# Performance work log

Hardware: AMD Instinct MI355X
Metric: run time of the kernel (lower is better)

Reference implementation:

```python
import jax, jax.numpy as jnp
import numpy as np

B, T, IMG = 64, 20, 64
IN_DIM = IMG * IMG          # 4096, from x.view(B,-1,64*64)
C_IN = 8                    # input_channels
R_DIM = C_IN * 1024         # 8192, reshape(B,20,-1,32,32) constraint
NF = 64                     # num_filters
Z_DIM = 256
LIN_IN = 2 * NF * 7 * 7     # 6272


def setup_inputs() -> dict:
    key = jax.random.key(0)
    ks = jax.random.split(key, 10)
    x = jax.random.normal(ks[0], (B, T, IMG, IMG), jnp.float32)
    Win = jax.random.normal(ks[1], (IN_DIM, R_DIM), jnp.float32) / np.sqrt(IN_DIM).astype(np.float32)
    U = jax.random.normal(ks[2], (IN_DIM, R_DIM), jnp.float32) / np.sqrt(IN_DIM).astype(np.float32)
    Wr = jax.random.normal(ks[3], (R_DIM, R_DIM), jnp.float32) / np.sqrt(R_DIM).astype(np.float32)
    conv1_w = jax.random.normal(ks[4], (NF, C_IN, 3, 3, 3), jnp.float32) * 0.05
    conv1_b = jax.random.normal(ks[5], (NF,), jnp.float32) * 0.01
    conv2_w = jax.random.normal(ks[6], (2 * NF, NF, 3, 4, 4), jnp.float32) * 0.05
    conv2_b = jax.random.normal(ks[7], (2 * NF,), jnp.float32) * 0.01
    lin_w = jax.random.normal(ks[8], (Z_DIM, LIN_IN), jnp.float32) * 0.02
    lin_b = jax.random.normal(ks[9], (Z_DIM,), jnp.float32) * 0.01
    return {"x": x, "Win": Win, "U": U, "Wr": Wr,
            "conv1_w": conv1_w, "conv1_b": conv1_b,
            "conv2_w": conv2_w, "conv2_b": conv2_b,
            "lin_w": lin_w, "lin_b": lin_b}


def reference(x, Win, U, Wr, conv1_w, conv1_b, conv2_w, conv2_b, lin_w, lin_b):
    Bn = x.shape[0]
    xf = x.reshape(Bn, T, IN_DIM)                      # (B,T,4096)
    h0 = jnp.tanh(xf[:, 0] @ Win)                      # (B,R)
    xU = jnp.einsum('bti,ir->tbr', xf[:, 1:], U)       # precompute input drive (T-1,B,R)

    def step(h, xu):
        h = jnp.tanh(xu + h @ Wr)
        return h, h

    _, hs = jax.lax.scan(step, h0, xU)                 # (T-1,B,R)
    H = jnp.concatenate([h0[None], hs], axis=0)        # (T,B,R)
    H = jnp.swapaxes(H, 0, 1)                          # (B,T,R)

    h = H.reshape(Bn, T, C_IN, 32, 32).transpose(0, 2, 1, 3, 4)  # (B,C,T,32,32)
    dn = ('NCDHW', 'OIDHW', 'NCDHW')
    y = jax.lax.conv_general_dilated(h, conv1_w, (1, 2, 2),
                                     [(1, 1), (1, 1), (1, 1)], dimension_numbers=dn)
    y = y + conv1_b[None, :, None, None, None]
    y = jax.nn.leaky_relu(y, 0.01)                     # (B,NF,20,16,16)
    y = jax.lax.conv_general_dilated(y, conv2_w, (1, 2, 2),
                                     [(1, 1), (0, 0), (0, 0)], dimension_numbers=dn)
    y = y + conv2_b[None, :, None, None, None]
    y = jax.nn.leaky_relu(y, 0.01)                     # (B,2NF,20,7,7)

    y = y.reshape(Bn, -1, T, LIN_IN)                   # (B,1,20,6272), same row-major view as torch
    y = y @ lin_w.T + lin_b                            # (B,1,20,Z_DIM)
    mu, log_var = jnp.split(y, 2, axis=3)
    return mu, log_var
```

## Files before the change

kernel.cpp:

```cpp
#include <hip/hip_runtime.h>

typedef __bf16 v8bf __attribute__((ext_vector_type(8)));
typedef float  v4f  __attribute__((ext_vector_type(4)));
typedef unsigned short us8 __attribute__((ext_vector_type(8)));

__device__ __forceinline__ float bf2f(unsigned short u) {
    union { unsigned int i; float f; } v; v.i = ((unsigned int)u) << 16; return v.f;
}
__device__ __forceinline__ unsigned short f2bf(float f) {
    union { float f; unsigned int i; } v; v.f = f;
    return (unsigned short)((v.i + 0x7fffu + ((v.i >> 16) & 1u)) >> 16);
}
__device__ __forceinline__ int sw(int b) { return b ^ (((b >> 7) & 7) << 4); }

__global__ __launch_bounds__(256)
void transpose_f32_bf16(const float* __restrict__ src,
                        unsigned short* __restrict__ dst, int K, int N)
{
    __shared__ unsigned short tile[64][72];
    const int tid = threadIdx.x;
    const int c0 = blockIdx.x * 64, r0 = blockIdx.y * 64;
    const int tr = tid >> 2, tc4 = tid & 3;
    const float* sp = src + (size_t)(r0 + tr) * N + c0 + tc4 * 16;
#pragma unroll
    for (int j = 0; j < 4; ++j) {
        v4f f = *reinterpret_cast<const v4f*>(sp + j * 4);
#pragma unroll
        for (int e = 0; e < 4; ++e) tile[tr][tc4 * 16 + j * 4 + e] = f2bf(f[e]);
    }
    __syncthreads();
    const int ow = tid >> 3, och = tid & 7;
#pragma unroll
    for (int p = 0; p < 2; ++p) {
        int orow = p * 32 + ow;
        us8 o;
#pragma unroll
        for (int e = 0; e < 8; ++e) o[e] = tile[och * 8 + e][orow];
        *reinterpret_cast<us8*>(dst + (size_t)(c0 + orow) * K + r0 + och * 8) = o;
    }
}

__global__ __launch_bounds__(256)
void cvt_x(const float* __restrict__ x, unsigned short* __restrict__ xb)
{
    int i = blockIdx.x * 256 + threadIdx.x;
    if (i >= 655360) return;
    v4f f0 = *reinterpret_cast<const v4f*>(x + (size_t)i * 8);
    v4f f1 = *reinterpret_cast<const v4f*>(x + (size_t)i * 8 + 4);
    us8 o;
#pragma unroll
    for (int e = 0; e < 4; ++e) { o[e] = f2bf(f0[e]); o[4 + e] = f2bf(f1[e]); }
    *reinterpret_cast<us8*>(xb + (size_t)i * 8) = o;
}

template<int BN, bool STORE_BF16, bool AF32, bool BF32>
__global__ __launch_bounds__(256, 2)
void gemm_bt(const void* __restrict__ Ap, int lda_lo, int lda_hi,
             const void* __restrict__ BTp, int ldb,
             void* __restrict__ Cout, int ldc,
             int ksub, long long csplit_stride)
{
    constexpr int FN  = BN / 32;
    constexpr int BCH = BN / 32;
    const int tid = threadIdx.x;
    const int lane = tid & 63, wid = tid >> 6;
    const int wr = wid >> 1, wc = wid & 1;
    const int nt = blockIdx.x, mt = blockIdx.y, kz = blockIdx.z;
    const int n0 = nt * BN;
    const int kstart = kz * ksub;

    __shared__ unsigned short smem[(64 + BN) * 64];
    char* As = reinterpret_cast<char*>(smem);
    char* Bs = reinterpret_cast<char*>(smem + 64 * 64);

    const unsigned short* A16 = (const unsigned short*)Ap;
    const float*          A32 = (const float*)Ap;
    const unsigned short* B16 = (const unsigned short*)BTp;
    const float*          B32 = (const float*)BTp;

    const int arow = AF32 ? (tid >> 2) : (tid >> 3);
    const int aq   = AF32 ? (tid & 3) : (tid & 7);
    const float* Ab32 = A32 + (size_t)arow * lda_lo + (size_t)mt * lda_hi + kstart + aq * 16;
    const unsigned short* Ab16 = A16 + (size_t)arow * lda_lo + (size_t)mt * lda_hi + kstart + aq * 8;
    const int brow = tid >> 3, bq = tid & 7;
    const float* Bb32 = B32 + (size_t)(n0 + brow) * ldb + kstart + bq * 8;
    const unsigned short* Bb16 = B16 + (size_t)(n0 + brow) * ldb + kstart + bq * 8;

    v4f fa[4];
    us8 ra[2];
    v4f fb[BCH][2];
    us8 rb[BCH];

    auto load = [&](int kk) {
        if (AF32) {
#pragma unroll
            for (int j = 0; j < 4; ++j)
                fa[j] = *reinterpret_cast<const v4f*>(Ab32 + kk + j * 4);
        } else {
#pragma unroll
            for (int p = 0; p < 2; ++p)
                ra[p] = *reinterpret_cast<const us8*>(Ab16 + (size_t)(p * 32) * lda_lo + kk);
        }
        if (BF32) {
#pragma unroll
            for (int p = 0; p < BCH; ++p) {
                fb[p][0] = *reinterpret_cast<const v4f*>(Bb32 + (size_t)(p * 32) * ldb + kk);
                fb[p][1] = *reinterpret_cast<const v4f*>(Bb32 + (size_t)(p * 32) * ldb + kk + 4);
            }
        } else {
#pragma unroll
            for (int p = 0; p < BCH; ++p)
                rb[p] = *reinterpret_cast<const us8*>(Bb16 + (size_t)(p * 32) * ldb + kk);
        }
    };
    auto stage = [&]() {
        if (AF32) {
#pragma unroll
            for (int h = 0; h < 2; ++h) {
                us8 v;
#pragma unroll
                for (int e = 0; e < 8; ++e) v[e] = f2bf(fa[h * 2 + (e >> 2)][e & 3]);
                *reinterpret_cast<us8*>(As + arow * 128 + (((aq * 2 + h) * 16) ^ ((arow & 7) << 4))) = v;
            }
        } else {
#pragma unroll
            for (int p = 0; p < 2; ++p)
                *reinterpret_cast<us8*>(As + (arow + p * 32) * 128 + ((aq * 16) ^ ((arow & 7) << 4))) = ra[p];
        }
#pragma unroll
        for (int p = 0; p < BCH; ++p) {
            us8 v;
            if (BF32) {
#pragma unroll
                for (int e = 0; e < 8; ++e) v[e] = f2bf(fb[p][e >> 2][e & 3]);
            } else v = rb[p];
            *reinterpret_cast<us8*>(Bs + (brow + p * 32) * 128 + ((bq * 16) ^ ((brow & 7) << 4))) = v;
        }
    };

    v4f z4 = {0.f, 0.f, 0.f, 0.f};
    v4f acc[2][FN];
#pragma unroll
    for (int i = 0; i < 2; ++i)
#pragma unroll
        for (int j = 0; j < FN; ++j) acc[i][j] = z4;

    const int l15 = lane & 15, l4 = lane >> 4;
    const int nk = ksub / 64;
    load(0);
    for (int it = 0; it < nk; ++it) {
        __syncthreads();
        stage();
        __syncthreads();
        if (it + 1 < nk) load((it + 1) * 64);
#pragma unroll
        for (int ks = 0; ks < 2; ++ks) {
            const int kb = (ks * 32 + l4 * 8) * 2;
            v8bf af[2], bfr[FN];
#pragma unroll
            for (int fm = 0; fm < 2; ++fm) {
                int row = wr * 32 + fm * 16 + l15;
                af[fm] = *reinterpret_cast<const v8bf*>(As + row * 128 + (kb ^ ((row & 7) << 4)));
            }
#pragma unroll
            for (int fn = 0; fn < FN; ++fn) {
                int row = wc * (BN / 2) + fn * 16 + l15;
                bfr[fn] = *reinterpret_cast<const v8bf*>(Bs + row * 128 + (kb ^ ((row & 7) << 4)));
            }
#pragma unroll
            for (int fm = 0; fm < 2; ++fm)
#pragma unroll
                for (int fn = 0; fn < FN; ++fn)
                    acc[fm][fn] = __builtin_amdgcn_mfma_f32_16x16x32_bf16(af[fm], bfr[fn], acc[fm][fn], 0, 0, 0);
        }
    }
    const long long m0 = (long long)mt * 64;
#pragma unroll
    for (int fm = 0; fm < 2; ++fm)
#pragma unroll
        for (int fn = 0; fn < FN; ++fn)
#pragma unroll
            for (int r = 0; r < 4; ++r) {
                long long row = m0 + wr * 32 + fm * 16 + l4 * 4 + r;
                long long col = n0 + wc * (BN / 2) + fn * 16 + l15;
                long long idx = (long long)kz * csplit_stride + row * ldc + col;
                if (STORE_BF16) reinterpret_cast<unsigned short*>(Cout)[idx] = f2bf(acc[fm][fn][r]);
                else            reinterpret_cast<float*>(Cout)[idx]          = acc[fm][fn][r];
            }
}

#define KZ 4
__global__ __launch_bounds__(256, 2)
void scan_step(const unsigned short* __restrict__ A, int lda,
               const unsigned short* __restrict__ BT, int ldb,
               int kper,
               const unsigned short* __restrict__ xu,
               unsigned short* __restrict__ hnext,
               unsigned short* __restrict__ Hbf, int t,
               float* __restrict__ part,
               unsigned int* __restrict__ tickets)
{
    const int tid = threadIdx.x, lane = tid & 63, wid = tid >> 6;
    const int wr = wid >> 1, wc = wid & 1;
    const int nt = blockIdx.x & 127, kz = blockIdx.x >> 7;
    const int n0 = nt * 64, kstart = kz * kper;
    const int l15 = lane & 15, l4 = lane >> 4;
    const int nit = kper >> 6;

    __shared__ unsigned short smem[32768];
    char* base = reinterpret_cast<char*>(smem);

    const int srow = tid >> 3, sq = tid & 7;
    const int gslot = sq ^ (srow & 7);
    const unsigned short* Asrc = A + (size_t)srow * lda + kstart + gslot * 8;
    const unsigned short* Bsrc = BT + (size_t)(n0 + srow) * ldb + kstart + gslot * 8;

    auto stage = [&](int buf, int kk) {
        char* dA = base + buf * 16384 + wid * 1024;
        char* dB = dA + 8192;
#pragma unroll
        for (int p = 0; p < 2; ++p) {
            __builtin_amdgcn_global_load_lds(
                (const __attribute__((address_space(1))) void*)(Asrc + kk + (size_t)p * 32 * lda),
                (__attribute__((address_space(3))) void*)(dA + p * 4096), 16, 0, 0);
            __builtin_amdgcn_global_load_lds(
                (const __attribute__((address_space(1))) void*)(Bsrc + kk + (size_t)p * 32 * ldb),
                (__attribute__((address_space(3))) void*)(dB + p * 4096), 16, 0, 0);
        }
    };

    v4f acc00 = {0.f, 0.f, 0.f, 0.f};
    v4f acc01 = acc00, acc10 = acc00, acc11 = acc00;

    stage(0, 0); stage(1, 64); stage(2, 128);
    for (int it = 0; it < nit; ++it) {
        const int ahead = nit - 1 - it;
        if (ahead >= 2)      asm volatile("s_waitcnt vmcnt(8)" ::: "memory");
        else if (ahead == 1) asm volatile("s_waitcnt vmcnt(4)" ::: "memory");
        else                 asm volatile("s_waitcnt vmcnt(0)" ::: "memory");
        __builtin_amdgcn_s_barrier();
        __builtin_amdgcn_sched_barrier(0);
        if (it + 3 < nit) stage((it + 3) & 3, (it + 3) * 64);
        const char* As = base + (it & 3) * 16384;
        const char* Bs = As + 8192;
#pragma unroll
        for (int ks = 0; ks < 2; ++ks) {
            const int kb = (ks * 32 + l4 * 8) * 2;
            v8bf a0, a1, b0, b1;
            { int row = wr * 32 + l15;      a0 = *reinterpret_cast<const v8bf*>(As + row * 128 + (kb ^ ((row & 7) << 4))); }
            { int row = wr * 32 + 16 + l15; a1 = *reinterpret_cast<const v8bf*>(As + row * 128 + (kb ^ ((row & 7) << 4))); }
            { int row = wc * 32 + l15;      b0 = *reinterpret_cast<const v8bf*>(Bs + row * 128 + (kb ^ ((row & 7) << 4))); }
            { int row = wc * 32 + 16 + l15; b1 = *reinterpret_cast<const v8bf*>(Bs + row * 128 + (kb ^ ((row & 7) << 4))); }
            acc00 = __builtin_amdgcn_mfma_f32_16x16x32_bf16(a0, b0, acc00, 0, 0, 0);
            acc01 = __builtin_amdgcn_mfma_f32_16x16x32_bf16(a0, b1, acc01, 0, 0, 0);
            acc10 = __builtin_amdgcn_mfma_f32_16x16x32_bf16(a1, b0, acc10, 0, 0, 0);
            acc11 = __builtin_amdgcn_mfma_f32_16x16x32_bf16(a1, b1, acc11, 0, 0, 0);
        }
    }

    float* mypart = part + (size_t)kz * 524288;
#pragma unroll
    for (int r = 0; r < 4; ++r) {
        int row0 = wr * 32 + l4 * 4 + r;
        int col0 = n0 + wc * 32 + l15;
        mypart[(size_t)row0 * 8192 + col0]             = acc00[r];
        mypart[(size_t)row0 * 8192 + col0 + 16]        = acc01[r];
        mypart[(size_t)(row0 + 16) * 8192 + col0]      = acc10[r];
        mypart[(size_t)(row0 + 16) * 8192 + col0 + 16] = acc11[r];
    }

    __shared__ int lastflag;
    __syncthreads();
    if (tid == 0) {
        unsigned int old = __hip_atomic_fetch_add(&tickets[nt], 1u,
                              __ATOMIC_ACQ_REL, __HIP_MEMORY_SCOPE_AGENT);
        lastflag = (old == KZ - 1);
    }
    __syncthreads();
    if (!lastflag) return;

    const int row = tid >> 2;
    const int c0 = n0 + (tid & 3) * 16;
    float pre[16];
    if (xu) {
        const us8* xp = reinterpret_cast<const us8*>(xu + (size_t)row * 8192 + c0);
        us8 x0 = xp[0], x1 = xp[1];
#pragma unroll
        for (int j = 0; j < 8; ++j) { pre[j] = bf2f(x0[j]); pre[8 + j] = bf2f(x1[j]); }
    } else {
#pragma unroll
        for (int j = 0; j < 16; ++j) pre[j] = 0.f;
    }
#pragma unroll
    for (int z = 0; z < KZ; ++z) {
        const float* pp = part + (size_t)z * 524288 + (size_t)row * 8192 + c0;
#pragma unroll
        for (int q = 0; q < 4; ++q) {
            v4f v = *reinterpret_cast<const v4f*>(pp + q * 4);
#pragma unroll
            for (int e = 0; e < 4; ++e) pre[q * 4 + e] += v[e];
        }
    }
    us8 o0, o1;
#pragma unroll
    for (int j = 0; j < 16; ++j) {
        unsigned short hb = f2bf(tanhf(pre[j]));
        if (j < 8) o0[j] = hb; else o1[j - 8] = hb;
        int col = c0 + j;
        Hbf[(((size_t)row * 20 + t) * 1024 + (col & 1023)) * 8 + (col >> 10)] = hb;
    }
    *reinterpret_cast<us8*>(hnext + (size_t)row * 8192 + c0)     = o0;
    *reinterpret_cast<us8*>(hnext + (size_t)row * 8192 + c0 + 8) = o1;
    if (tid == 0)
        __hip_atomic_store(&tickets[nt], 0u, __ATOMIC_RELAXED, __HIP_MEMORY_SCOPE_AGENT);
}

__global__ __launch_bounds__(256)
void cvt_w1(const float* __restrict__ w, unsigned short* __restrict__ o,
            unsigned int* __restrict__ tickets)
{
    if (blockIdx.x == 0 && threadIdx.x < 128) tickets[threadIdx.x] = 0;
    int idx = blockIdx.x * 256 + threadIdx.x;
    if (idx >= 64 * 224) return;
    int co = idx / 224, k = idx % 224;
    int g = k >> 3, ci = k & 7;
    float v = 0.f;
    if (g < 27) {
        int dt = g / 9, rr = g % 9, dy = rr / 3, dx = rr % 3;
        v = w[(((co * 8 + ci) * 3 + dt) * 3 + dy) * 3 + dx];
    }
    o[idx] = f2bf(v);
}
__global__ __launch_bounds__(256)
void cvt_w2(const float* __restrict__ w, unsigned short* __restrict__ o)
{
    int idx = blockIdx.x * 256 + threadIdx.x;
    if (idx >= 128 * 3072) return;
    int co = idx / 3072, k = idx % 3072;
    int g = k >> 6, ci = k & 63;
    int dt = g >> 4, dy = (g >> 2) & 3, dx = g & 3;
    o[idx] = f2bf(w[(((co * 64 + ci) * 3 + dt) * 4 + dy) * 4 + dx]);
}

__global__ __launch_bounds__(256, 2)
void conv1_kernel(const unsigned short* __restrict__ H,
                  const unsigned short* __restrict__ w1,
                  const float* __restrict__ bias,
                  unsigned short* __restrict__ y1)
{
    const int b = blockIdx.x, t = blockIdx.y;
    const int tid = threadIdx.x, lane = tid & 63, wid = tid >> 6;
    __shared__ unsigned short in_s[3 * 33 * 33 * 8];
    __shared__ unsigned short w_s[64 * 224];

    for (int i = tid; i < 13068; i += 256) reinterpret_cast<unsigned int*>(in_s)[i] = 0;
    __syncthreads();
    for (int idx = tid; idx < 3 * 1024; idx += 256) {
        int dt = idx >> 10, rem = idx & 1023;
        int iy = rem >> 5, ix = rem & 31;
        int ts = t + dt - 1;
        if (ts >= 0 && ts < 20) {
            us8 v = *reinterpret_cast<const us8*>(H + (((size_t)b * 20 + ts) * 1024 + rem) * 8);
            int byte = ((dt * 33 + iy + 1) * 33 + (ix + 1)) * 16;
            *reinterpret_cast<us8*>(reinterpret_cast<char*>(in_s) + sw(byte)) = v;
        }
    }
    for (int idx = tid; idx < 64 * 28; idx += 256) {
        int co = idx / 28, j = idx % 28;
        us8 v = *reinterpret_cast<const us8*>(w1 + co * 224 + j * 8);
        *reinterpret_cast<us8*>(reinterpret_cast<char*>(w_s) + sw(co * 448 + j * 16)) = v;
    }
    __syncthreads();

    const int l15 = lane & 15, l4 = lane >> 4;
    const int m_lo = wid * 64 + l15;
    v4f z4 = {0.f, 0.f, 0.f, 0.f};
    v4f acc[4][4];
#pragma unroll
    for (int i = 0; i < 4; ++i)
#pragma unroll
        for (int j = 0; j < 4; ++j) acc[i][j] = z4;

#pragma unroll
    for (int ks = 0; ks < 7; ++ks) {
        int g = ks * 4 + l4;
        int gc = g < 27 ? g : 26;
        int dt = gc / 9, rr = gc % 9, dy = rr / 3, dx = rr % 3;
        v8bf ap[4], aw[4];
#pragma unroll
        for (int fm = 0; fm < 4; ++fm) {
            int m = fm * 16 + m_lo;
            int py = m >> 4, px = m & 15;
            int byte = ((dt * 33 + 2 * py + dy) * 33 + 2 * px + dx) * 16;
            ap[fm] = *reinterpret_cast<const v8bf*>(reinterpret_cast<const char*>(in_s) + sw(byte));
        }
        int kb2 = (ks * 32 + l4 * 8) * 2;
#pragma unroll
        for (int fc = 0; fc < 4; ++fc) {
            int co = fc * 16 + l15;
            aw[fc] = *reinterpret_cast<const v8bf*>(reinterpret_cast<const char*>(w_s) + sw(co * 448 + kb2));
        }
#pragma unroll
        for (int fm = 0; fm < 4; ++fm)
#pragma unroll
            for (int fc = 0; fc < 4; ++fc)
                acc[fm][fc] = __builtin_amdgcn_mfma_f32_16x16x32_bf16(ap[fm], aw[fc], acc[fm][fc], 0, 0, 0);
    }
#pragma unroll
    for (int fm = 0; fm < 4; ++fm)
#pragma unroll
        for (int fc = 0; fc < 4; ++fc)
#pragma unroll
            for (int r = 0; r < 4; ++r) {
                int m  = wid * 64 + fm * 16 + l4 * 4 + r;
                int co = fc * 16 + l15;
                float v = acc[fm][fc][r] + bias[co];
                v = v > 0.f ? v : 0.01f * v;
                y1[(((size_t)b * 20 + t) * 256 + m) * 64 + co] = f2bf(v);
            }
}

__global__ __launch_bounds__(512, 2)
void conv2_kernel(const unsigned short* __restrict__ y1,
                  const unsigned short* __restrict__ w2,
                  const float* __restrict__ bias,
                  unsigned short* __restrict__ y2)
{
    const int b = blockIdx.x, t = blockIdx.y;
    const int tid = threadIdx.x, lane = tid & 63, wid = tid >> 6;
    const int wc = wid >> 1, wr = wid & 1;
    __shared__ unsigned short in_s[256 * 64];
    __shared__ unsigned short w_s[128 * 128];
    const int l15 = lane & 15, l4 = lane >> 4;

    const int m0v = wr * 32 + l15, m1v = m0v + 16;
    const int m0c = m0v < 49 ? m0v : 48, m1c = m1v < 49 ? m1v : 48;
    const int py0 = m0c / 7, px0 = m0c - py0 * 7;
    const int py1 = m1c / 7, px1 = m1c - py1 * 7;

    v4f acc[2][2];
#pragma unroll
    for (int i = 0; i < 2; ++i)
#pragma unroll
        for (int j = 0; j < 2; ++j) acc[i][j] = (v4f){0.f, 0.f, 0.f, 0.f};

    for (int dt = 0; dt < 3; ++dt) {
        int ts = t + dt - 1;
        __syncthreads();
        if (ts < 0 || ts >= 20) continue;
#pragma unroll
        for (int p = 0; p < 4; ++p) {
            int idx = tid + p * 512;
            int slot = idx >> 3, c8 = idx & 7;
            int yy = slot >> 4, xx = slot & 15;
            us8 v = *reinterpret_cast<const us8*>(y1 + (((size_t)b * 20 + ts) * 256 + slot) * 64 + c8 * 8);
            int cell = ((yy & 1) * 2 + (xx & 1)) * 64 + (yy >> 1) * 8 + (xx >> 1);
            int byte = cell * 128 + ((c8 * 16) ^ (((cell ^ (cell >> 3)) & 7) << 4));
            *reinterpret_cast<us8*>(reinterpret_cast<char*>(in_s) + byte) = v;
        }
        for (int kc = 0; kc < 8; ++kc) {
            __syncthreads();
#pragma unroll
            for (int p = 0; p < 4; ++p) {
                int idx = tid + p * 512;
                int co = idx >> 4, j = idx & 15;
                us8 v = *reinterpret_cast<const us8*>(w2 + (size_t)co * 3072 + dt * 1024 + kc * 128 + j * 8);
                *reinterpret_cast<us8*>(reinterpret_cast<char*>(w_s) + co * 256 + ((j * 16) ^ ((co & 7) << 4))) = v;
            }
            __syncthreads();
#pragma unroll
            for (int ks = 0; ks < 4; ++ks) {
                int klocal = ks * 32 + l4 * 8;
                int kk = kc * 128 + klocal;
                int dy = (kk >> 8) & 3, dx = (kk >> 6) & 3, ci0 = kk & 63;
                v8bf aw[2], bp[2];
#pragma unroll
                for (int fc = 0; fc < 2; ++fc) {
                    int co = wc * 32 + fc * 16 + l15;
                    aw[fc] = *reinterpret_cast<const v8bf*>(reinterpret_cast<const char*>(w_s)
                               + co * 256 + ((klocal * 2) ^ ((co & 7) << 4)));
                }
                int plane = ((dy & 1) << 1) | (dx & 1);
                int c0 = plane * 64 + (py0 + (dy >> 1)) * 8 + px0 + (dx >> 1);
                int c1 = plane * 64 + (py1 + (dy >> 1)) * 8 + px1 + (dx >> 1);
                bp[0] = *reinterpret_cast<const v8bf*>(reinterpret_cast<const char*>(in_s)
                          + c0 * 128 + ((ci0 * 2) ^ (((c0 ^ (c0 >> 3)) & 7) << 4)));
                bp[1] = *reinterpret_cast<const v8bf*>(reinterpret_cast<const char*>(in_s)
                          + c1 * 128 + ((ci0 * 2) ^ (((c1 ^ (c1 >> 3)) & 7) << 4)));
#pragma unroll
                for (int fc = 0; fc < 2; ++fc)
#pragma unroll
                    for (int fm = 0; fm < 2; ++fm)
                        acc[fc][fm] = __builtin_amdgcn_mfma_f32_16x16x32_bf16(aw[fc], bp[fm], acc[fc][fm], 0, 0, 0);
            }
        }
    }
#pragma unroll
    for (int fc = 0; fc < 2; ++fc)
#pragma unroll
        for (int fm = 0; fm < 2; ++fm)
#pragma unroll
            for (int r = 0; r < 4; ++r) {
                int co = wc * 32 + fc * 16 + l4 * 4 + r;
                int m  = wr * 32 + fm * 16 + l15;
                if (m < 49) {
                    float v = acc[fc][fm][r] + bias[co];
                    v = v > 0.f ? v : 0.01f * v;
                    y2[(((size_t)b * 128 + co) * 20 + t) * 49 + m] = f2bf(v);
                }
            }
}

__global__ __launch_bounds__(256)
void lin_epi(const float* __restrict__ linC, const float* __restrict__ lb,
             float* __restrict__ out)
{
    int i = blockIdx.x * 256 + threadIdx.x;
    int m = i >> 8, n = i & 255;
    float v = lb[n];
#pragma unroll
    for (int z = 0; z < 7; ++z) v += linC[(size_t)z * 327680 + i];
    size_t o = (n < 128) ? ((size_t)m * 128 + n) : (163840 + (size_t)m * 128 + (n - 128));
    out[o] = v;
}

extern "C" void kernel_launch(void* const* d_in, const int* in_sizes, int n_in,
                              void* d_out, int out_size, void* d_ws, size_t ws_size,
                              hipStream_t stream)
{
    const float* x   = (const float*)d_in[0];
    const float* Win = (const float*)d_in[1];
    const float* U   = (const float*)d_in[2];
    const float* Wr  = (const float*)d_in[3];
    const float* c1w = (const float*)d_in[4];
    const float* c1b = (const float*)d_in[5];
    const float* c2w = (const float*)d_in[6];
    const float* c2b = (const float*)d_in[7];
    const float* lw  = (const float*)d_in[8];
    const float* lb  = (const float*)d_in[9];

    char* ws = (char*)d_ws;
    unsigned short* WrT  = (unsigned short*)(ws);
    unsigned short* xbf  = (unsigned short*)(ws);
    unsigned short* WT   = (unsigned short*)(ws + 134217728ll);
    unsigned short* y1   = (unsigned short*)(ws + 134217728ll);
    unsigned short* y2   = (unsigned short*)(ws + 176160768ll);
    unsigned short* XALL = (unsigned short*)(ws + 201326592ll);
    unsigned short* Hbf  = (unsigned short*)(ws + 222298112ll);
    unsigned short* hb0  = (unsigned short*)(ws + 243269632ll);
    unsigned short* hb1  = (unsigned short*)(ws + 244318208ll);
    float*          part = (float*)        (ws + 245366784ll);
    float*          linC = (float*)        (ws + 245366784ll);
    unsigned short* w1bf = (unsigned short*)(ws + 254541824ll);
    unsigned short* w2bf = (unsigned short*)(ws + 254570496ll);
    unsigned int*   tick = (unsigned int*) (ws + 255356928ll);
    float*          out  = (float*)d_out;

    cvt_w1<<<56, 256, 0, stream>>>(c1w, w1bf, tick);
    cvt_w2<<<1536, 256, 0, stream>>>(c2w, w2bf);
    cvt_x<<<2560, 256, 0, stream>>>(x, xbf);

    transpose_f32_bf16<<<dim3(128, 64), 256, 0, stream>>>(Win, WT, 4096, 8192);
    scan_step<<<512, 256, 0, stream>>>(xbf, 81920, WT, 4096, 1024,
                                       (const unsigned short*)nullptr, hb0, Hbf, 0, part, tick);

    transpose_f32_bf16<<<dim3(128, 64), 256, 0, stream>>>(U, WT, 4096, 8192);
    gemm_bt<128, true, true, false><<<dim3(64, 19, 1), 256, 0, stream>>>(
        x + 4096, 81920, 4096, WT, 4096, XALL + 524288, 8192, 4096, 0ll);

    transpose_f32_bf16<<<dim3(128, 128), 256, 0, stream>>>(Wr, WrT, 8192, 8192);
    for (int t = 1; t < 20; ++t) {
        const unsigned short* hprev = (t & 1) ? hb0 : hb1;
        unsigned short*       hnext = (t & 1) ? hb1 : hb0;
        scan_step<<<512, 256, 0, stream>>>(hprev, 8192, WrT, 8192, 2048,
                                           XALL + (size_t)t * 524288, hnext, Hbf, t, part, tick);
    }

    conv1_kernel<<<dim3(64, 20), 256, 0, stream>>>(Hbf, w1bf, c1b, y1);
    conv2_kernel<<<dim3(64, 20), 512, 0, stream>>>(y1, w2bf, c2b, y2);

    gemm_bt<128, false, false, true><<<dim3(2, 20, 7), 256, 0, stream>>>(
        y2, 6272, 6272 * 64, lw, 6272, linC, 256, 896, 327680ll);
    lin_epi<<<1280, 256, 0, stream>>>(linC, lb, out);
}
```

Measured before the change: 1.487 ms.

## Fuse recurrent scan steps into one persistent kernel with grid barriers

Replaces the 19 per-timestep scan_step launches with a single persistent scan_loop kernel of 512 blocks. Each timestep's split-K partial GEMM and its tanh reduction are separated by a software grid barrier built on an atomic counter and a generation word. The aim is to remove per-launch overhead and the ticket-based reduction. It also swaps the grid x/y order for the input-drive GEMM so neighbouring blocks share B tiles. Correctness depends on all 512 blocks being co-resident, otherwise the barrier deadlocks, and the tanh reduction now runs as a separate phase between two barriers.

Measured after the change: 1.877 ms. 26.2% more time.

```diff
diff --git a/kernel.cpp b/kernel.cpp
--- a/kernel.cpp
+++ b/kernel.cpp
@@ -12,6 +12,26 @@
     return (unsigned short)((v.i + 0x7fffu + ((v.i >> 16) & 1u)) >> 16);
 }
 __device__ __forceinline__ int sw(int b) { return b ^ (((b >> 7) & 7) << 4); }
+
+#define SCAN_BLOCKS 512
+__device__ __forceinline__ void gbar(unsigned int* bar) {
+    __syncthreads();
+    if (threadIdx.x == 0) {
+        unsigned int* cnt = bar;
+        unsigned int* gen = bar + 32;
+        unsigned int g = __hip_atomic_load(gen, __ATOMIC_RELAXED, __HIP_MEMORY_SCOPE_AGENT);
+        unsigned int a = __hip_atomic_fetch_add(cnt, 1u, __ATOMIC_ACQ_REL, __HIP_MEMORY_SCOPE_AGENT);
+        if (a == SCAN_BLOCKS - 1) {
+            __hip_atomic_store(cnt, 0u, __ATOMIC_RELAXED, __HIP_MEMORY_SCOPE_AGENT);
+            __hip_atomic_fetch_add(gen, 1u, __ATOMIC_RELEASE, __HIP_MEMORY_SCOPE_AGENT);
+        } else {
+            while (__hip_atomic_load(gen, __ATOMIC_RELAXED, __HIP_MEMORY_SCOPE_AGENT) == g)
+                __builtin_amdgcn_s_sleep(4);
+            (void)__hip_atomic_load(gen, __ATOMIC_ACQUIRE, __HIP_MEMORY_SCOPE_AGENT);
+        }
+    }
+    __syncthreads();
+}
 
 __global__ __launch_bounds__(256)
 void transpose_f32_bf16(const float* __restrict__ src,
@@ -53,7 +73,7 @@
     *reinterpret_cast<us8*>(xb + (size_t)i * 8) = o;
 }
 
-template<int BN, bool STORE_BF16, bool AF32, bool BF32>
+template<int BN, bool STORE_BF16, bool AF32, bool BF32, bool SWAPXY>
 __global__ __launch_bounds__(256, 2)
 void gemm_bt(const void* __restrict__ Ap, int lda_lo, int lda_hi,
              const void* __restrict__ BTp, int ldb,
@@ -65,7 +85,9 @@
     const int tid = threadIdx.x;
     const int lane = tid & 63, wid = tid >> 6;
     const int wr = wid >> 1, wc = wid & 1;
-    const int nt = blockIdx.x, mt = blockIdx.y, kz = blockIdx.z;
+    const int nt = SWAPXY ? blockIdx.y : blockIdx.x;
+    const int mt = SWAPXY ? blockIdx.x : blockIdx.y;
+    const int kz = blockIdx.z;
     const int n0 = nt * BN;
     const int kstart = kz * ksub;
 
@@ -315,11 +337,113 @@
         __hip_atomic_store(&tickets[nt], 0u, __ATOMIC_RELAXED, __HIP_MEMORY_SCOPE_AGENT);
 }
 
+__global__ __launch_bounds__(256, 2)
+void scan_loop(const unsigned short* __restrict__ WrT,
+               const unsigned short* __restrict__ xall,
+               unsigned short* __restrict__ hb0,
+               unsigned short* __restrict__ hb1,
+               unsigned short* __restrict__ Hbf,
+               float* __restrict__ part,
+               unsigned int* __restrict__ bar)
+{
+    const int tid = threadIdx.x, lane = tid & 63, wid = tid >> 6;
+    const int wr = wid >> 1, wc = wid & 1;
+    const int nt = blockIdx.x & 127, kz = blockIdx.x >> 7;
+    const int n0 = nt * 64, kstart = kz * 2048;
+    const int l15 = lane & 15, l4 = lane >> 4;
+
+    __shared__ unsigned short smem[32768];
+    char* base = reinterpret_cast<char*>(smem);
+
+    const int srow = tid >> 3, sq = tid & 7;
+    const int gslot = sq ^ (srow & 7);
+    const unsigned short* Bsrc = WrT + (size_t)(n0 + srow) * 8192 + kstart + gslot * 8;
+    const size_t aoff = (size_t)srow * 8192 + kstart + gslot * 8;
+    const int ci = blockIdx.x * 256 + tid;
+    float* mypart = part + (size_t)kz * 524288;
+
+    for (int t = 1; t < 20; ++t) {
+        const unsigned short* hprev = (t & 1) ? hb0 : hb1;
+        unsigned short*       hnext = (t & 1) ? hb1 : hb0;
+        const unsigned short* Asrc = hprev + aoff;
+
+        auto stage = [&](int buf, int kk) {
+            char* dA = base + buf * 16384 + wid * 1024;
+            char* dB = dA + 8192;
+#pragma unroll
+            for (int p = 0; p < 2; ++p) {
+                __builtin_amdgcn_global_load_lds(
+                    (const __attribute__((address_space(1))) void*)(Asrc + kk + (size_t)p * 32 * 8192),
+                    (__attribute__((address_space(3))) void*)(dA + p * 4096), 16, 0, 0);
+                __builtin_amdgcn_global_load_lds(
+                    (const __attribute__((address_space(1))) void*)(Bsrc + kk + (size_t)p * 32 * 8192),
+                    (__attribute__((address_space(3))) void*)(dB + p * 4096), 16, 0, 0);
+            }
+        };
+
+        v4f acc00 = {0.f, 0.f, 0.f, 0.f};
+        v4f acc01 = acc00, acc10 = acc00, acc11 = acc00;
+
+        stage(0, 0); stage(1, 64); stage(2, 128);
+        for (int it = 0; it < 32; ++it) {
+            const int ahead = 31 - it;
+            if (ahead >= 2)      asm volatile("s_waitcnt vmcnt(8)" ::: "memory");
+            else if (ahead == 1) asm volatile("s_waitcnt vmcnt(4)" ::: "memory");
+            else                 asm volatile("s_waitcnt vmcnt(0)" ::: "memory");
+            __builtin_amdgcn_s_barrier();
+            __builtin_amdgcn_sched_barrier(0);
+            if (it + 3 < 32) stage((it + 3) & 3, (it + 3) * 64);
+            const char* As = base + (it & 3) * 16384;
+            const char* Bs = As + 8192;
+#pragma unroll
+            for (int ks = 0; ks < 2; ++ks) {
+                const int kb = (ks * 32 + l4 * 8) * 2;
+                v8bf a0, a1, b0, b1;
+                { int row = wr * 32 + l15;      a0 = *reinterpret_cast<const v8bf*>(As + row * 128 + (kb ^ ((row & 7) << 4))); }
+                { int row = wr * 32 + 16 + l15; a1 = *reinterpret_cast<const v8bf*>(As + row * 128 + (kb ^ ((row & 7) << 4))); }
+                { int row = wc * 32 + l15;      b0 = *reinterpret_cast<const v8bf*>(Bs + row * 128 + (kb ^ ((row & 7) << 4))); }
+                { int row = wc * 32 + 16 + l15; b1 = *reinterpret_cast<const v8bf*>(Bs + row * 128 + (kb ^ ((row & 7) << 4))); }
+                acc00 = __builtin_amdgcn_mfma_f32_16x16x32_bf16(a0, b0, acc00, 0, 0, 0);
+                acc01 = __builtin_amdgcn_mfma_f32_16x16x32_bf16(a0, b1, acc01, 0, 0, 0);
+                acc10 = __builtin_amdgcn_mfma_f32_16x16x32_bf16(a1, b0, acc10, 0, 0, 0);
+                acc11 = __builtin_amdgcn_mfma_f32_16x16x32_bf16(a1, b1, acc11, 0, 0, 0);
+            }
+        }
+
+#pragma unroll
+        for (int r = 0; r < 4; ++r) {
+            int row0 = wr * 32 + l4 * 4 + r;
+            int col0 = n0 + wc * 32 + l15;
+            mypart[(size_t)row0 * 8192 + col0]             = acc00[r];
+            mypart[(size_t)row0 * 8192 + col0 + 16]        = acc01[r];
+            mypart[(size_t)(row0 + 16) * 8192 + col0]      = acc10[r];
+            mypart[(size_t)(row0 + 16) * 8192 + col0 + 16] = acc11[r];
+        }
+        gbar(bar);
+
+        const unsigned short* xu = xall + (size_t)t * 524288;
+#pragma unroll
+        for (int j = 0; j < 4; ++j) {
+            int i = ci + j * 131072;
+            float pre = bf2f(xu[i]);
+#pragma unroll
+            for (int z = 0; z < 4; ++z) pre += part[(size_t)z * 524288 + i];
+            unsigned short hb = f2bf(tanhf(pre));
+            hnext[i] = hb;
+            int b = i >> 13, r2 = i & 8191;
+            int c = r2 >> 10, pp = r2 & 1023;
+            Hbf[(((size_t)b * 20 + t) * 1024 + pp) * 8 + c] = hb;
+        }
+        gbar(bar);
+    }
+}
+
 __global__ __launch_bounds__(256)
 void cvt_w1(const float* __restrict__ w, unsigned short* __restrict__ o,
-            unsigned int* __restrict__ tickets)
+            unsigned int* __restrict__ tickets, unsigned int* __restrict__ bar)
 {
     if (blockIdx.x == 0 && threadIdx.x < 128) tickets[threadIdx.x] = 0;
+    if (blockIdx.x == 0 && threadIdx.x < 64)  bar[threadIdx.x] = 0;
     int idx = blockIdx.x * 256 + threadIdx.x;
     if (idx >= 64 * 224) return;
     int co = idx / 224, k = idx % 224;
@@ -554,9 +678,10 @@
     unsigned short* w1bf = (unsigned short*)(ws + 254541824ll);
     unsigned short* w2bf = (unsigned short*)(ws + 254570496ll);
     unsigned int*   tick = (unsigned int*) (ws + 255356928ll);
+    unsigned int*   bar  = (unsigned int*) (ws + 255357440ll);
     float*          out  = (float*)d_out;
 
-    cvt_w1<<<56, 256, 0, stream>>>(c1w, w1bf, tick);
+    cvt_w1<<<56, 256, 0, stream>>>(c1w, w1bf, tick, bar);
     cvt_w2<<<1536, 256, 0, stream>>>(c2w, w2bf);
     cvt_x<<<2560, 256, 0, stream>>>(x, xbf);
 
@@ -565,21 +690,16 @@
                                        (const unsigned short*)nullptr, hb0, Hbf, 0, part, tick);
 
     transpose_f32_bf16<<<dim3(128, 64), 256, 0, stream>>>(U, WT, 4096, 8192);
-    gemm_bt<128, true, true, false><<<dim3(64, 19, 1), 256, 0, stream>>>(
+    gemm_bt<128, true, true, false, true><<<dim3(19, 64, 1), 256, 0, stream>>>(
         x + 4096, 81920, 4096, WT, 4096, XALL + 524288, 8192, 4096, 0ll);
 
     transpose_f32_bf16<<<dim3(128, 128), 256, 0, stream>>>(Wr, WrT, 8192, 8192);
-    for (int t = 1; t < 20; ++t) {
-        const unsigned short* hprev = (t & 1) ? hb0 : hb1;
-        unsigned short*       hnext = (t & 1) ? hb1 : hb0;
-        scan_step<<<512, 256, 0, stream>>>(hprev, 8192, WrT, 8192, 2048,
-                                           XALL + (size_t)t * 524288, hnext, Hbf, t, part, tick);
-    }
+    scan_loop<<<SCAN_BLOCKS, 256, 0, stream>>>(WrT, XALL, hb0, hb1, Hbf, part, bar);
 
     conv1_kernel<<<dim3(64, 20), 256, 0, stream>>>(Hbf, w1bf, c1b, y1);
     conv2_kernel<<<dim3(64, 20), 512, 0, stream>>>(y1, w2bf, c2b, y2);
 
-    gemm_bt<128, false, false, true><<<dim3(2, 20, 7), 256, 0, stream>>>(
+    gemm_bt<128, false, false, true, false><<<dim3(2, 20, 7), 256, 0, stream>>>(
         y2, 6272, 6272 * 64, lw, 6272, linC, 256, 896, 327680ll);
     lin_epi<<<1280, 256, 0, stream>>>(linC, lb, out);
 }
```

## Pre-tile and swizzle recurrent weights so scan loads are contiguous 8KB blocks

Applied to the files above, without the earlier changes.

Adds a transpose kernel that writes Win and Wr into 64x64 bf16 tiles, already XOR-swizzled, stored contiguously per (n-tile, k-tile). The scan_step B-operand loads then read one contiguous 8KB block per stage instead of 64 strided rows, which should improve DRAM/L2 access efficiency in the 20 bandwidth-bound recurrent steps. It also swaps the grid axes of the U projection GEMM so consecutive blocks share the same N tile of weights. The tiled layout couples the transpose kernel and scan_step tightly.

New measurement: 1.549 ms. 1.04x slower.

```diff
diff --git a/kernel.cpp b/kernel.cpp
--- a/kernel.cpp
+++ b/kernel.cpp
@@ -41,6 +41,34 @@
 }
 
 __global__ __launch_bounds__(256)
+void transpose_f32_bf16_tiled(const float* __restrict__ src,
+                              unsigned short* __restrict__ dst, int N, int ktiles)
+{
+    __shared__ unsigned short tile[64][72];
+    const int tid = threadIdx.x;
+    const int c0 = blockIdx.x * 64, r0 = blockIdx.y * 64;
+    const int tr = tid >> 2, tc4 = tid & 3;
+    const float* sp = src + (size_t)(r0 + tr) * N + c0 + tc4 * 16;
+#pragma unroll
+    for (int j = 0; j < 4; ++j) {
+        v4f f = *reinterpret_cast<const v4f*>(sp + j * 4);
+#pragma unroll
+        for (int e = 0; e < 4; ++e) tile[tr][tc4 * 16 + j * 4 + e] = f2bf(f[e]);
+    }
+    __syncthreads();
+    const int ow = tid >> 3, och = tid & 7;
+    unsigned short* tb = dst + ((size_t)blockIdx.x * ktiles + blockIdx.y) * 4096;
+#pragma unroll
+    for (int p = 0; p < 2; ++p) {
+        int orow = p * 32 + ow;
+        us8 o;
+#pragma unroll
+        for (int e = 0; e < 8; ++e) o[e] = tile[och * 8 + e][orow];
+        *reinterpret_cast<us8*>(tb + orow * 64 + (och ^ (orow & 7)) * 8) = o;
+    }
+}
+
+__global__ __launch_bounds__(256)
 void cvt_x(const float* __restrict__ x, unsigned short* __restrict__ xb)
 {
     int i = blockIdx.x * 256 + threadIdx.x;
@@ -53,7 +81,7 @@
     *reinterpret_cast<us8*>(xb + (size_t)i * 8) = o;
 }
 
-template<int BN, bool STORE_BF16, bool AF32, bool BF32>
+template<int BN, bool STORE_BF16, bool AF32, bool BF32, bool SWAPXY>
 __global__ __launch_bounds__(256, 2)
 void gemm_bt(const void* __restrict__ Ap, int lda_lo, int lda_hi,
              const void* __restrict__ BTp, int ldb,
@@ -65,7 +93,9 @@
     const int tid = threadIdx.x;
     const int lane = tid & 63, wid = tid >> 6;
     const int wr = wid >> 1, wc = wid & 1;
-    const int nt = blockIdx.x, mt = blockIdx.y, kz = blockIdx.z;
+    const int nt = SWAPXY ? blockIdx.y : blockIdx.x;
+    const int mt = SWAPXY ? blockIdx.x : blockIdx.y;
+    const int kz = blockIdx.z;
     const int n0 = nt * BN;
     const int kstart = kz * ksub;
 
@@ -192,7 +222,7 @@
 #define KZ 4
 __global__ __launch_bounds__(256, 2)
 void scan_step(const unsigned short* __restrict__ A, int lda,
-               const unsigned short* __restrict__ BT, int ldb,
+               const unsigned short* __restrict__ BTiles, int ktiles,
                int kper,
                const unsigned short* __restrict__ xu,
                unsigned short* __restrict__ hnext,
@@ -213,18 +243,20 @@
     const int srow = tid >> 3, sq = tid & 7;
     const int gslot = sq ^ (srow & 7);
     const unsigned short* Asrc = A + (size_t)srow * lda + kstart + gslot * 8;
-    const unsigned short* Bsrc = BT + (size_t)(n0 + srow) * ldb + kstart + gslot * 8;
-
-    auto stage = [&](int buf, int kk) {
+    const unsigned short* Bsrc = BTiles
+        + ((size_t)(nt * ktiles + kz * (kper >> 6))) * 4096 + tid * 8;
+
+    auto stage = [&](int buf, int it) {
         char* dA = base + buf * 16384 + wid * 1024;
         char* dB = dA + 8192;
+        const int kk = it * 64;
 #pragma unroll
         for (int p = 0; p < 2; ++p) {
             __builtin_amdgcn_global_load_lds(
                 (const __attribute__((address_space(1))) void*)(Asrc + kk + (size_t)p * 32 * lda),
                 (__attribute__((address_space(3))) void*)(dA + p * 4096), 16, 0, 0);
             __builtin_amdgcn_global_load_lds(
-                (const __attribute__((address_space(1))) void*)(Bsrc + kk + (size_t)p * 32 * ldb),
+                (const __attribute__((address_space(1))) void*)(Bsrc + (size_t)it * 4096 + p * 2048),
                 (__attribute__((address_space(3))) void*)(dB + p * 4096), 16, 0, 0);
         }
     };
@@ -232,7 +264,7 @@
     v4f acc00 = {0.f, 0.f, 0.f, 0.f};
     v4f acc01 = acc00, acc10 = acc00, acc11 = acc00;
 
-    stage(0, 0); stage(1, 64); stage(2, 128);
+    stage(0, 0); stage(1, 1); stage(2, 2);
     for (int it = 0; it < nit; ++it) {
         const int ahead = nit - 1 - it;
         if (ahead >= 2)      asm volatile("s_waitcnt vmcnt(8)" ::: "memory");
@@ -240,7 +272,7 @@
         else                 asm volatile("s_waitcnt vmcnt(0)" ::: "memory");
         __builtin_amdgcn_s_barrier();
         __builtin_amdgcn_sched_barrier(0);
-        if (it + 3 < nit) stage((it + 3) & 3, (it + 3) * 64);
+        if (it + 3 < nit) stage((it + 3) & 3, it + 3);
         const char* As = base + (it & 3) * 16384;
         const char* Bs = As + 8192;
 #pragma unroll
@@ -540,7 +572,7 @@
     const float* lb  = (const float*)d_in[9];
 
     char* ws = (char*)d_ws;
-    unsigned short* WrT  = (unsigned short*)(ws);
+    unsigned short* WrTile = (unsigned short*)(ws);
     unsigned short* xbf  = (unsigned short*)(ws);
     unsigned short* WT   = (unsigned short*)(ws + 134217728ll);
     unsigned short* y1   = (unsigned short*)(ws + 134217728ll);
@@ -560,26 +592,26 @@
     cvt_w2<<<1536, 256, 0, stream>>>(c2w, w2bf);
     cvt_x<<<2560, 256, 0, stream>>>(x, xbf);
 
-    transpose_f32_bf16<<<dim3(128, 64), 256, 0, stream>>>(Win, WT, 4096, 8192);
-    scan_step<<<512, 256, 0, stream>>>(xbf, 81920, WT, 4096, 1024,
+    transpose_f32_bf16_tiled<<<dim3(128, 64), 256, 0, stream>>>(Win, WT, 8192, 64);
+    scan_step<<<512, 256, 0, stream>>>(xbf, 81920, WT, 64, 1024,
                                        (const unsigned short*)nullptr, hb0, Hbf, 0, part, tick);
 
     transpose_f32_bf16<<<dim3(128, 64), 256, 0, stream>>>(U, WT, 4096, 8192);
-    gemm_bt<128, true, true, false><<<dim3(64, 19, 1), 256, 0, stream>>>(
+    gemm_bt<128, true, true, false, true><<<dim3(19, 64, 1), 256, 0, stream>>>(
         x + 4096, 81920, 4096, WT, 4096, XALL + 524288, 8192, 4096, 0ll);
 
-    transpose_f32_bf16<<<dim3(128, 128), 256, 0, stream>>>(Wr, WrT, 8192, 8192);
+    transpose_f32_bf16_tiled<<<dim3(128, 128), 256, 0, stream>>>(Wr, WrTile, 8192, 128);
     for (int t = 1; t < 20; ++t) {
         const unsigned short* hprev = (t & 1) ? hb0 : hb1;
         unsigned short*       hnext = (t & 1) ? hb1 : hb0;
-        scan_step<<<512, 256, 0, stream>>>(hprev, 8192, WrT, 8192, 2048,
+        scan_step<<<512, 256, 0, stream>>>(hprev, 8192, WrTile, 128, 2048,
                                            XALL + (size_t)t * 524288, hnext, Hbf, t, part, tick);
     }
 
     conv1_kernel<<<dim3(64, 20), 256, 0, stream>>>(Hbf, w1bf, c1b, y1);
     conv2_kernel<<<dim3(64, 20), 512, 0, stream>>>(y1, w2bf, c2b, y2);
 
-    gemm_bt<128, false, false, true><<<dim3(2, 20, 7), 256, 0, stream>>>(
+    gemm_bt<128, false, false, true, false><<<dim3(2, 20, 7), 256, 0, stream>>>(
         y2, 6272, 6272 * 64, lw, 6272, linC, 256, 896, 327680ll);
     lin_epi<<<1280, 256, 0, stream>>>(linC, lb, out);
 }
```
